# Performance work log

Hardware: AMD Instinct MI355X
Metric: run time of the kernel (lower is better)

The kernel has to match this reference:

```python
import jax, jax.numpy as jnp
import numpy as np

B, S, E, H = 2, 2048, 1024, 16
D = E // H  # head_dim = 64
FE = 4      # forward_expansion
EPS = 1e-5


def layernorm(x, g, b):
    mu = jnp.mean(x, axis=-1, keepdims=True)
    var = jnp.var(x, axis=-1, keepdims=True)
    return (x - mu) * jax.lax.rsqrt(var + EPS) * g + b


def setup_inputs() -> dict:
    key = jax.random.key(0)
    ks = jax.random.split(key, 16)
    s = lambda d: 1.0 / np.sqrt(d)
    return {
        "queries": jax.random.normal(ks[0], (B, S, E), jnp.float32),
        "keys": jax.random.normal(ks[1], (B, S, E), jnp.float32),
        "values": jax.random.normal(ks[2], (B, S, E), jnp.float32),
        "mask": jnp.ones((B, 1, S, S), jnp.int32),  # ignored (faithful to source bug)
        "Wq": jax.random.normal(ks[3], (D, D), jnp.float32) * s(D),
        "Wk": jax.random.normal(ks[4], (D, D), jnp.float32) * s(D),
        "Wv": jax.random.normal(ks[5], (D, D), jnp.float32) * s(D),
        "Wfc": jax.random.normal(ks[6], (E, E), jnp.float32) * s(E),
        "bfc": jnp.zeros((E,), jnp.float32),
        "W1": jax.random.normal(ks[7], (FE * E, E), jnp.float32) * s(E),
        "b1": jnp.zeros((FE * E,), jnp.float32),
        "W2": jax.random.normal(ks[8], (E, FE * E), jnp.float32) * s(FE * E),
        "b2": jnp.zeros((E,), jnp.float32),
        "ln1_g": jnp.ones((E,), jnp.float32),
        "ln1_b": jnp.zeros((E,), jnp.float32),
        "ln2_g": jnp.ones((E,), jnp.float32),
        "ln2_b": jnp.zeros((E,), jnp.float32),
    }


def reference(queries, keys, values, mask, Wq, Wk, Wv, Wfc, bfc, W1, b1, W2, b2,
              ln1_g, ln1_b, ln2_g, ln2_b):
    # --- MHA ---
    q = queries.reshape(B, S, H, D) @ Wq.T  # [B,S,H,D]
    k = keys.reshape(B, S, H, D) @ Wk.T
    v = values.reshape(B, S, H, D) @ Wv.T
    scores = jnp.einsum('bqhd,bkhd->bhqk', q, k)
    # source: softmax(scores / S**(-1/2)) == scores * sqrt(S)  (faithful quirk)
    # mask is ignored: source masked_fill is non-inplace and discarded
    attn = jax.nn.softmax(scores * jnp.sqrt(jnp.float32(S)), axis=-1)
    out = jnp.einsum('bhqk,bkhd->bqhd', attn, v).reshape(B, S, E)
    att = out @ Wfc.T + bfc
    # --- residual + LN + FFN + LN (dropout p=0 -> identity) ---
    h = layernorm(att + queries, ln1_g, ln1_b)
    x = jax.nn.relu(h @ W1.T + b1) @ W2.T + b2
    return layernorm(x + h, ln2_g, ln2_b)
```

## Files before the change

kernel.cpp:

```cpp
#include <hip/hip_runtime.h>
#include <hip/hip_bf16.h>
#include <math.h>

#define B_ 2
#define S_ 2048
#define E_ 1024
#define H_ 16
#define D_ 64
#define TOK (B_*S_)
#define SCALE 45.254833995939045f
#define SCALE2 (45.254833995939045f * 1.44269504088896340f)

typedef __bf16 bf16x8 __attribute__((ext_vector_type(8)));
typedef float floatx4 __attribute__((ext_vector_type(4)));
struct b4s { __hip_bfloat16 x, y, z, w; };

typedef const __attribute__((address_space(1))) char ga_char;
typedef __attribute__((address_space(3))) char ls_char;

__device__ __forceinline__ void gload_lds16(const void* g, ls_char* l) {
  __builtin_amdgcn_global_load_lds((ga_char*)g, l, 16, 0, 0);
}

#if __has_builtin(__builtin_amdgcn_exp2f)
#define EXP2(x) __builtin_amdgcn_exp2f(x)
#else
#define EXP2(x) exp2f(x)
#endif

#define SWZ(arr, half, row, qpos) \
  (*(bf16x8*)&arr[half][row][(((qpos) ^ ((row) & 3)) * 8)])

__device__ __forceinline__ int fsw(int r) {
  return ((r >> 3) & 1) | ((((r >> 4) ^ (r >> 2)) & 1) << 1);
}
#define SWZ2(arr, half, row, qpos) \
  (*(bf16x8*)&arr[half][row][(((qpos) ^ fsw(row)) * 8)])

__global__ __launch_bounds__(256) void cast_all(
    const float* __restrict__ Wfc, const float* __restrict__ W1,
    const float* __restrict__ W2, __hip_bfloat16* __restrict__ Wfcb,
    __hip_bfloat16* __restrict__ W1b, __hip_bfloat16* __restrict__ W2b,
    const float* __restrict__ Wq, const float* __restrict__ Wk,
    const float* __restrict__ Wv, __hip_bfloat16* __restrict__ Whl) {
  const int i = blockIdx.x * 256 + threadIdx.x;
  if (i < 2359296) {
    const float* src; __hip_bfloat16* dst; int j;
    if (i < 262144)       { src = Wfc; dst = Wfcb; j = i; }
    else if (i < 1310720) { src = W1;  dst = W1b;  j = i - 262144; }
    else                  { src = W2;  dst = W2b;  j = i - 1310720; }
    float4 v = ((const float4*)src)[j];
    b4s o;
    o.x = __float2bfloat16(v.x); o.y = __float2bfloat16(v.y);
    o.z = __float2bfloat16(v.z); o.w = __float2bfloat16(v.w);
    *(b4s*)(dst + (size_t)j * 4) = o;
  } else if (i < 2362368) {
    const int idx = i - 2359296;
    const int m = idx >> 10;
    const int off = (idx & 1023) * 4;
    const float* W = (m == 0) ? Wq : (m == 1) ? Wk : Wv;
    float4 v = *(const float4*)(W + off);
    b4s hi, lo;
    hi.x = __float2bfloat16(v.x); lo.x = __float2bfloat16(v.x - __bfloat162float(hi.x));
    hi.y = __float2bfloat16(v.y); lo.y = __float2bfloat16(v.y - __bfloat162float(hi.y));
    hi.z = __float2bfloat16(v.z); lo.z = __float2bfloat16(v.z - __bfloat162float(hi.z));
    hi.w = __float2bfloat16(v.w); lo.w = __float2bfloat16(v.w - __bfloat162float(hi.w));
    *(b4s*)(Whl + (size_t)m * 8192 + off) = hi;
    *(b4s*)(Whl + (size_t)m * 8192 + 4096 + off) = lo;
  }
}

__global__ __launch_bounds__(256) void qkv_fused(
    const float* __restrict__ xq, const float* __restrict__ xk,
    const float* __restrict__ xv, const __hip_bfloat16* __restrict__ Whl,
    __hip_bfloat16* __restrict__ qhi, __hip_bfloat16* __restrict__ qlo,
    __hip_bfloat16* __restrict__ khi, __hip_bfloat16* __restrict__ klo,
    __hip_bfloat16* __restrict__ vt) {
  __shared__ __bf16 Xh[2][64][32], Xl[2][64][32];
  __shared__ __bf16 Vt[64][72];
  const int t = threadIdx.x, lane = t & 63, w = t >> 6;
  const int quad = lane >> 4, low = lane & 15;
  const int bh = blockIdx.y;
  const int b = bh >> 4, h = bh & 15;
  const int s0 = blockIdx.x * 64;
  const int sr = t >> 2;
  const int sc = (t & 3) * 16;
  const int scc = sc >> 5;
  const int p0 = (sc & 31) >> 3;

  for (int m = 0; m < 3; m++) {
    const float* xin = (m == 0) ? xq : (m == 1) ? xk : xv;
    const __hip_bfloat16* Wh = Whl + (size_t)m * 8192;
    const float sc_m = (m == 0) ? SCALE2 : 1.0f;

    __syncthreads();
    {
      const float* src = xin + ((size_t)(b * S_ + s0 + sr)) * E_ + h * 64 + sc;
      float4 f0 = *(const float4*)(src);
      float4 f1 = *(const float4*)(src + 4);
      float4 f2 = *(const float4*)(src + 8);
      float4 f3 = *(const float4*)(src + 12);
      float fv[16] = {f0.x, f0.y, f0.z, f0.w, f1.x, f1.y, f1.z, f1.w,
                      f2.x, f2.y, f2.z, f2.w, f3.x, f3.y, f3.z, f3.w};
      bf16x8 hi0, hi1, lo0, lo1;
      #pragma unroll
      for (int j = 0; j < 8; j++) {
        hi0[j] = (__bf16)fv[j];
        lo0[j] = (__bf16)(fv[j] - (float)hi0[j]);
        hi1[j] = (__bf16)fv[8 + j];
        lo1[j] = (__bf16)(fv[8 + j] - (float)hi1[j]);
      }
      SWZ(Xh, scc, sr, p0) = hi0;
      SWZ(Xh, scc, sr, p0 + 1) = hi1;
      SWZ(Xl, scc, sr, p0) = lo0;
      SWZ(Xl, scc, sr, p0 + 1) = lo1;
    }
    __syncthreads();

    bf16x8 ah[2], al[2];
    #pragma unroll
    for (int c = 0; c < 2; c++) {
      ah[c] = SWZ(Xh, c, w * 16 + low, quad);
      al[c] = SWZ(Xl, c, w * 16 + low, quad);
    }

    floatx4 acc[4];
    #pragma unroll
    for (int nn = 0; nn < 4; nn++) {
      floatx4 a = {};
      #pragma unroll
      for (int c = 0; c < 2; c++) {
        const __hip_bfloat16* wp = Wh + (nn * 16 + low) * 64 + c * 32 + quad * 8;
        bf16x8 wh_ = *(const bf16x8*)wp;
        bf16x8 wl_ = *(const bf16x8*)(wp + 4096);
        a = __builtin_amdgcn_mfma_f32_16x16x32_bf16(ah[c], wh_, a, 0, 0, 0);
        a = __builtin_amdgcn_mfma_f32_16x16x32_bf16(al[c], wh_, a, 0, 0, 0);
        a = __builtin_amdgcn_mfma_f32_16x16x32_bf16(ah[c], wl_, a, 0, 0, 0);
      }
      acc[nn] = a;
    }

    if (m < 2) {
      __hip_bfloat16* dh = (m == 0) ? qhi : khi;
      __hip_bfloat16* dl = (m == 0) ? qlo : klo;
      #pragma unroll
      for (int nn = 0; nn < 4; nn++) {
        #pragma unroll
        for (int i = 0; i < 4; i++) {
          const int s = s0 + w * 16 + quad * 4 + i;
          const int d = nn * 16 + low;
          const size_t adr = ((size_t)bh * S_ + s) * 64 + d;
          const float f = acc[nn][i] * sc_m;
          const __hip_bfloat16 hb = __float2bfloat16(f);
          dh[adr] = hb;
          dl[adr] = __float2bfloat16(f - __bfloat162float(hb));
        }
      }
    } else {
      #pragma unroll
      for (int nn = 0; nn < 4; nn++)
        #pragma unroll
        for (int i = 0; i < 4; i++)
          Vt[nn * 16 + low][w * 16 + quad * 4 + i] = (__bf16)acc[nn][i];
      __syncthreads();
      const int dr = t >> 2;
      const int scl = (t & 3) * 16;
      __hip_bfloat16* dst = vt + ((size_t)bh * 64 + dr) * S_ + s0 + scl;
      bf16x8 o0 = *(const bf16x8*)&Vt[dr][scl];
      bf16x8 o1 = *(const bf16x8*)&Vt[dr][scl + 8];
      *(bf16x8*)dst = o0;
      *(bf16x8*)(dst + 8) = o1;
    }
  }
}

__global__ __launch_bounds__(512, 4) void attn_mfma(
    const __hip_bfloat16* __restrict__ Qhi, const __hip_bfloat16* __restrict__ Qlo,
    const __hip_bfloat16* __restrict__ Khi, const __hip_bfloat16* __restrict__ Klo,
    const __hip_bfloat16* __restrict__ Vtg, __hip_bfloat16* __restrict__ ctx) {
  __shared__ __bf16 Kh[2][2][64][32], Kl[2][2][64][32], Vs[2][2][64][32];
  const int t = threadIdx.x, lane = t & 63, w = t >> 6;
  const int quad = lane >> 4, low = lane & 15;
  const int bh = blockIdx.x;
  const int qw = blockIdx.y * 128 + w * 16;

  const int sh = w >> 2;
  const int r0 = (w & 3) * 16;
  const int srow = r0 + (lane >> 2);
  const int sq = (lane & 3) ^ fsw(srow);
  const __hip_bfloat16* gK = Khi + ((size_t)bh * S_ + srow) * 64 + sh * 32 + sq * 8;
  const __hip_bfloat16* gL = Klo + ((size_t)bh * S_ + srow) * 64 + sh * 32 + sq * 8;
  const __hip_bfloat16* gV = Vtg + ((size_t)bh * 64 + srow) * S_ + sh * 32 + sq * 8;

  bf16x8 qh[2], ql[2];
  {
    const size_t qbase = ((size_t)bh * S_ + qw + low) * 64 + quad * 8;
    qh[0] = *(const bf16x8*)(Qhi + qbase);
    qh[1] = *(const bf16x8*)(Qhi + qbase + 32);
    ql[0] = *(const bf16x8*)(Qlo + qbase);
    ql[1] = *(const bf16x8*)(Qlo + qbase + 32);
  }

  floatx4 oacc[4] = {};
  float mrow = -3e38f, lrow = 0.f;

  gload_lds16(gK, (ls_char*)&Kh[0][sh][r0][0]);
  gload_lds16(gL, (ls_char*)&Kl[0][sh][r0][0]);
  gload_lds16(gV, (ls_char*)&Vs[0][sh][r0][0]);

  for (int kt = 0; kt < S_ / 64; kt++) {
    const int cur = kt & 1;
    __syncthreads();
    if (kt + 1 < S_ / 64) {
      gload_lds16(gK + (size_t)(kt + 1) * 4096, (ls_char*)&Kh[cur ^ 1][sh][r0][0]);
      gload_lds16(gL + (size_t)(kt + 1) * 4096, (ls_char*)&Kl[cur ^ 1][sh][r0][0]);
      gload_lds16(gV + (size_t)(kt + 1) * 64,   (ls_char*)&Vs[cur ^ 1][sh][r0][0]);
    }

    floatx4 sa[4];
    #pragma unroll
    for (int nn = 0; nn < 4; nn++) {
      const int prow = (nn & 1) * 32 + (nn >> 1) * 4 + (low >> 2) * 8 + (low & 3);
      bf16x8 kh0 = SWZ2(Kh[cur], 0, prow, quad);
      bf16x8 kh1 = SWZ2(Kh[cur], 1, prow, quad);
      bf16x8 kl0 = SWZ2(Kl[cur], 0, prow, quad);
      bf16x8 kl1 = SWZ2(Kl[cur], 1, prow, quad);
      floatx4 s = {};
      s = __builtin_amdgcn_mfma_f32_16x16x32_bf16(kh0, qh[0], s, 0, 0, 0);
      s = __builtin_amdgcn_mfma_f32_16x16x32_bf16(kh1, qh[1], s, 0, 0, 0);
      s = __builtin_amdgcn_mfma_f32_16x16x32_bf16(kl0, qh[0], s, 0, 0, 0);
      s = __builtin_amdgcn_mfma_f32_16x16x32_bf16(kl1, qh[1], s, 0, 0, 0);
      s = __builtin_amdgcn_mfma_f32_16x16x32_bf16(kh0, ql[0], s, 0, 0, 0);
      s = __builtin_amdgcn_mfma_f32_16x16x32_bf16(kh1, ql[1], s, 0, 0, 0);
      sa[nn] = s;
    }

    float rmax;
    {
      float m0 = fmaxf(fmaxf(sa[0][0], sa[0][1]), fmaxf(sa[0][2], sa[0][3]));
      float m1 = fmaxf(fmaxf(sa[1][0], sa[1][1]), fmaxf(sa[1][2], sa[1][3]));
      float m2 = fmaxf(fmaxf(sa[2][0], sa[2][1]), fmaxf(sa[2][2], sa[2][3]));
      float m3 = fmaxf(fmaxf(sa[3][0], sa[3][1]), fmaxf(sa[3][2], sa[3][3]));
      rmax = fmaxf(fmaxf(m0, m1), fmaxf(m2, m3));
      rmax = fmaxf(rmax, __shfl_xor(rmax, 16, 64));
      rmax = fmaxf(rmax, __shfl_xor(rmax, 32, 64));
    }
    if (__any(rmax > mrow)) {
      const float nm = fmaxf(mrow, rmax);
      const float al = EXP2(mrow - nm);
      mrow = nm;
      lrow *= al;
      #pragma unroll
      for (int dt = 0; dt < 4; dt++) {
        oacc[dt][0] *= al; oacc[dt][1] *= al;
        oacc[dt][2] *= al; oacc[dt][3] *= al;
      }
    }
    float p[4][4];
    float rs;
    {
      float r0_ = 0.f, r1_ = 0.f, r2_ = 0.f, r3_ = 0.f;
      #pragma unroll
      for (int i = 0; i < 4; i++) {
        p[0][i] = EXP2(sa[0][i] - mrow); r0_ += p[0][i];
        p[1][i] = EXP2(sa[1][i] - mrow); r1_ += p[1][i];
        p[2][i] = EXP2(sa[2][i] - mrow); r2_ += p[2][i];
        p[3][i] = EXP2(sa[3][i] - mrow); r3_ += p[3][i];
      }
      rs = (r0_ + r1_) + (r2_ + r3_);
      rs += __shfl_xor(rs, 16, 64);
      rs += __shfl_xor(rs, 32, 64);
    }
    lrow += rs;

    bf16x8 pb[2];
    #pragma unroll
    for (int kh2 = 0; kh2 < 2; kh2++) {
      bf16x8 v;
      v[0] = (__bf16)p[kh2][0]; v[1] = (__bf16)p[kh2][1];
      v[2] = (__bf16)p[kh2][2]; v[3] = (__bf16)p[kh2][3];
      v[4] = (__bf16)p[kh2 + 2][0]; v[5] = (__bf16)p[kh2 + 2][1];
      v[6] = (__bf16)p[kh2 + 2][2]; v[7] = (__bf16)p[kh2 + 2][3];
      pb[kh2] = v;
    }

    #pragma unroll
    for (int dt = 0; dt < 4; dt++) {
      bf16x8 vb0 = SWZ2(Vs[cur], 0, dt * 16 + low, quad);
      bf16x8 vb1 = SWZ2(Vs[cur], 1, dt * 16 + low, quad);
      oacc[dt] = __builtin_amdgcn_mfma_f32_16x16x32_bf16(vb0, pb[0], oacc[dt], 0, 0, 0);
      oacc[dt] = __builtin_amdgcn_mfma_f32_16x16x32_bf16(vb1, pb[1], oacc[dt], 0, 0, 0);
    }
  }

  const float inv = 1.0f / lrow;
  const int b = bh >> 4, h = bh & 15;
  const size_t base = ((size_t)(b * S_ + qw + low)) * E_ + h * 64 + quad * 4;
  #pragma unroll
  for (int dt = 0; dt < 4; dt++) {
    b4s o;
    o.x = __float2bfloat16(oacc[dt][0] * inv);
    o.y = __float2bfloat16(oacc[dt][1] * inv);
    o.z = __float2bfloat16(oacc[dt][2] * inv);
    o.w = __float2bfloat16(oacc[dt][3] * inv);
    *(b4s*)(ctx + base + dt * 16) = o;
  }
}

template <int RELU, int OUT_BF16, int PARTIAL>
__global__ __launch_bounds__(256) void gemm_mfma(
    const __hip_bfloat16* __restrict__ A, const __hip_bfloat16* __restrict__ Wt,
    const float* __restrict__ bias, void* __restrict__ C0, void* __restrict__ C1,
    int M, int N, int Kblk, int lda) {
  __shared__ __bf16 As[128][64];
  __shared__ __bf16 Bs[128][64];
  const int t = threadIdx.x;
  const int lane = t & 63;
  const int w = t >> 6;
  const int wr = w >> 1, wc = w & 1;
  const int m0 = blockIdx.y * 128, n0 = blockIdx.x * 128;
  void* Cout = (blockIdx.z == 0) ? C0 : C1;

  A += (size_t)blockIdx.z * Kblk;
  Wt += (size_t)blockIdx.z * Kblk;

  floatx4 acc[4][4] = {};
  const int srow = t >> 3;
  const int ssc = ((t & 7) ^ (srow & 7)) * 8;

  const __hip_bfloat16* gA = A + (size_t)(m0 + srow) * lda + ssc;
  const __hip_bfloat16* gB = Wt + (size_t)(n0 + srow) * lda + ssc;
  ls_char* lA = (ls_char*)&As[0][0] + w * 1024;
  ls_char* lB = (ls_char*)&Bs[0][0] + w * 1024;
  const size_t rstep = (size_t)32 * lda;

  for (int k0 = 0; k0 < Kblk; k0 += 64) {
    __syncthreads();
    gload_lds16(gA + k0,             lA);
    gload_lds16(gA + k0 + rstep,     lA + 4096);
    gload_lds16(gA + k0 + 2 * rstep, lA + 8192);
    gload_lds16(gA + k0 + 3 * rstep, lA + 12288);
    gload_lds16(gB + k0,             lB);
    gload_lds16(gB + k0 + rstep,     lB + 4096);
    gload_lds16(gB + k0 + 2 * rstep, lB + 8192);
    gload_lds16(gB + k0 + 3 * rstep, lB + 12288);
    __syncthreads();

    #pragma unroll
    for (int ks = 0; ks < 2; ks++) {
      bf16x8 af[4], bfr[4];
      #pragma unroll
      for (int i = 0; i < 4; i++) {
        const int ra = wr * 64 + i * 16 + (lane & 15);
        const int ca = (((lane >> 4) + ks * 4) ^ (ra & 7)) * 8;
        af[i] = *(const bf16x8*)&As[ra][ca];
        const int rb = wc * 64 + i * 16 + (lane & 15);
        const int cb = (((lane >> 4) + ks * 4) ^ (rb & 7)) * 8;
        bfr[i] = *(const bf16x8*)&Bs[rb][cb];
      }
      #pragma unroll
      for (int mi = 0; mi < 4; mi++)
        #pragma unroll
        for (int ni = 0; ni < 4; ni++)
          acc[mi][ni] = __builtin_amdgcn_mfma_f32_16x16x32_bf16(
              af[mi], bfr[ni], acc[mi][ni], 0, 0, 0);
    }
  }

  const int cil = lane & 15;
  const int quad = lane >> 4;
  #pragma unroll
  for (int ni = 0; ni < 4; ni++) {
    const int col = n0 + wc * 64 + ni * 16 + cil;
    const float bb = PARTIAL ? 0.f : bias[col];
    #pragma unroll
    for (int mi = 0; mi < 4; mi++) {
      const int row = m0 + wr * 64 + mi * 16 + quad * 4;
      #pragma unroll
      for (int i = 0; i < 4; i++) {
        if (PARTIAL) {
          ((float*)Cout)[(size_t)(row + i) * N + col] = acc[mi][ni][i];
        } else {
          float vv = acc[mi][ni][i] + bb;
          if (RELU) vv = fmaxf(vv, 0.f);
          if (OUT_BF16)
            ((__hip_bfloat16*)Cout)[(size_t)(row + i) * N + col] = __float2bfloat16(vv);
          else
            ((float*)Cout)[(size_t)(row + i) * N + col] = vv;
        }
      }
    }
  }
}

template <int EMIT_BF16>
__global__ __launch_bounds__(256) void add_ln(
    const float* __restrict__ a0, const float* __restrict__ a1,
    const float* __restrict__ r, const float* __restrict__ bias,
    const float* __restrict__ g, const float* __restrict__ bt,
    float* __restrict__ out, __hip_bfloat16* __restrict__ outb) {
  __shared__ float red[16];
  const int tok = blockIdx.x, t = threadIdx.x;
  float4 av = ((const float4*)(a0 + (size_t)tok * E_))[t];
  float4 a2 = ((const float4*)(a1 + (size_t)tok * E_))[t];
  float4 rv = ((const float4*)(r + (size_t)tok * E_))[t];
  float4 cv = ((const float4*)bias)[t];
  float4 x;
  x.x = av.x + a2.x + rv.x + cv.x; x.y = av.y + a2.y + rv.y + cv.y;
  x.z = av.z + a2.z + rv.z + cv.z; x.w = av.w + a2.w + rv.w + cv.w;
  float sum = x.x + x.y + x.z + x.w;
  float ssq = x.x * x.x + x.y * x.y + x.z * x.z + x.w * x.w;
  #pragma unroll
  for (int off = 32; off >= 1; off >>= 1) {
    sum += __shfl_down(sum, off, 64);
    ssq += __shfl_down(ssq, off, 64);
  }
  const int wave = t >> 6;
  if ((t & 63) == 0) { red[wave] = sum; red[4 + wave] = ssq; }
  __syncthreads();
  if (t == 0) {
    float s = red[0] + red[1] + red[2] + red[3];
    float qq = red[4] + red[5] + red[6] + red[7];
    float mu = s * (1.0f / E_);
    red[8] = mu;
    red[9] = qq * (1.0f / E_) - mu * mu;
  }
  __syncthreads();
  const float mu = red[8];
  const float inv = rsqrtf(red[9] + 1e-5f);
  float4 gv = ((const float4*)g)[t];
  float4 bv = ((const float4*)bt)[t];
  float4 o;
  o.x = (x.x - mu) * inv * gv.x + bv.x;
  o.y = (x.y - mu) * inv * gv.y + bv.y;
  o.z = (x.z - mu) * inv * gv.z + bv.z;
  o.w = (x.w - mu) * inv * gv.w + bv.w;
  ((float4*)(out + (size_t)tok * E_))[t] = o;
  if (EMIT_BF16) {
    b4s ob;
    ob.x = __float2bfloat16(o.x); ob.y = __float2bfloat16(o.y);
    ob.z = __float2bfloat16(o.z); ob.w = __float2bfloat16(o.w);
    *(b4s*)(outb + (size_t)tok * E_ + t * 4) = ob;
  }
}

extern "C" void kernel_launch(void* const* d_in, const int* in_sizes, int n_in,
                              void* d_out, int out_size, void* d_ws, size_t ws_size,
                              hipStream_t stream) {
  const float* queries = (const float*)d_in[0];
  const float* keys    = (const float*)d_in[1];
  const float* values  = (const float*)d_in[2];
  const float* Wq  = (const float*)d_in[4];
  const float* Wk  = (const float*)d_in[5];
  const float* Wv  = (const float*)d_in[6];
  const float* Wfc = (const float*)d_in[7];
  const float* bfc = (const float*)d_in[8];
  const float* W1  = (const float*)d_in[9];
  const float* b1  = (const float*)d_in[10];
  const float* W2  = (const float*)d_in[11];
  const float* b2  = (const float*)d_in[12];
  const float* ln1_g = (const float*)d_in[13];
  const float* ln1_b = (const float*)d_in[14];
  const float* ln2_g = (const float*)d_in[15];
  const float* ln2_b = (const float*)d_in[16];

  const size_t M1 = 1048576;
  float* ws = (float*)d_ws;
  float* P0  = ws;
  float* P1  = ws + 4 * M1;
  float* Hf  = ws + 8 * M1;
  __hip_bfloat16* bb = (__hip_bfloat16*)(ws + 12 * M1);
  __hip_bfloat16* CTXb = bb;
  __hip_bfloat16* Hb   = bb + 4 * M1;
  __hip_bfloat16* Wfcb = bb + 8 * M1;
  __hip_bfloat16* W1b  = bb + 9 * M1;
  __hip_bfloat16* W2b  = bb + 13 * M1;
  __hip_bfloat16* Qhi  = bb + 17 * M1;
  __hip_bfloat16* Qlo  = bb + 21 * M1;
  __hip_bfloat16* Khi  = bb + 25 * M1;
  __hip_bfloat16* Klo  = bb + 29 * M1;
  __hip_bfloat16* Vtb  = bb + 33 * M1;
  __hip_bfloat16* FF1b = bb + 17 * M1;
  __hip_bfloat16* Whlb = bb + 37 * M1;
  float* out = (float*)d_out;

  cast_all<<<9228, 256, 0, stream>>>(Wfc, W1, W2, Wfcb, W1b, W2b,
                                     Wq, Wk, Wv, Whlb);

  qkv_fused<<<dim3(S_ / 64, B_ * H_), 256, 0, stream>>>(
      queries, keys, values, Whlb, Qhi, Qlo, Khi, Klo, Vtb);
  attn_mfma<<<dim3(B_ * H_, S_ / 128), 512, 0, stream>>>(
      Qhi, Qlo, Khi, Klo, Vtb, CTXb);
  gemm_mfma<0, 0, 1><<<dim3(E_ / 128, TOK / 128, 2), 256, 0, stream>>>(
      CTXb, Wfcb, nullptr, P0, P1, TOK, E_, 512, E_);
  add_ln<1><<<TOK, 256, 0, stream>>>(P0, P1, queries, bfc, ln1_g, ln1_b, Hf, Hb);
  gemm_mfma<1, 1, 0><<<dim3(4 * E_ / 128, TOK / 128, 1), 256, 0, stream>>>(
      Hb, W1b, b1, FF1b, FF1b, TOK, 4 * E_, E_, E_);
  gemm_mfma<0, 0, 1><<<dim3(E_ / 128, TOK / 128, 2), 256, 0, stream>>>(
      FF1b, W2b, nullptr, P0, P1, TOK, E_, 2048, 4 * E_);
  add_ln<0><<<TOK, 256, 0, stream>>>(P0, P1, Hf, b2, ln2_g, ln2_b, out, nullptr);
}
```

Baseline: 397.2 us.

## Add MFMA priority hints, simplify LDS swizzle, drop split-K for Wfc GEMM

The attention kernel raises wave priority around its MFMA blocks with s_setprio and moves the softmax into a helper. It also replaces the custom fsw LDS swizzle with the simpler row&3 XOR swizzle, which may bring back bank conflicts. The output-projection GEMM no longer uses split-K: it runs as one pass with bias fused in, so the first add_ln reads one partial instead of two plus bias. add_ln is templated to skip loads it does not need.

```diff
diff --git a/kernel.cpp b/kernel.cpp
--- a/kernel.cpp
+++ b/kernel.cpp
@@ -8,7 +8,6 @@
 #define H_ 16
 #define D_ 64
 #define TOK (B_*S_)
-#define SCALE 45.254833995939045f
 #define SCALE2 (45.254833995939045f * 1.44269504088896340f)
 
 typedef __bf16 bf16x8 __attribute__((ext_vector_type(8)));
@@ -30,12 +29,6 @@
 
 #define SWZ(arr, half, row, qpos) \
   (*(bf16x8*)&arr[half][row][(((qpos) ^ ((row) & 3)) * 8)])
-
-__device__ __forceinline__ int fsw(int r) {
-  return ((r >> 3) & 1) | ((((r >> 4) ^ (r >> 2)) & 1) << 1);
-}
-#define SWZ2(arr, half, row, qpos) \
-  (*(bf16x8*)&arr[half][row][(((qpos) ^ fsw(row)) * 8)])
 
 __global__ __launch_bounds__(256) void cast_all(
     const float* __restrict__ Wfc, const float* __restrict__ W1,
@@ -174,6 +167,56 @@
   }
 }
 
+__device__ __forceinline__ void softmax_update(
+    const floatx4* sa, floatx4* oacc, float& mrow, float& lrow, bf16x8* pb) {
+  float rmax;
+  {
+    float m0 = fmaxf(fmaxf(sa[0][0], sa[0][1]), fmaxf(sa[0][2], sa[0][3]));
+    float m1 = fmaxf(fmaxf(sa[1][0], sa[1][1]), fmaxf(sa[1][2], sa[1][3]));
+    float m2 = fmaxf(fmaxf(sa[2][0], sa[2][1]), fmaxf(sa[2][2], sa[2][3]));
+    float m3 = fmaxf(fmaxf(sa[3][0], sa[3][1]), fmaxf(sa[3][2], sa[3][3]));
+    rmax = fmaxf(fmaxf(m0, m1), fmaxf(m2, m3));
+    rmax = fmaxf(rmax, __shfl_xor(rmax, 16, 64));
+    rmax = fmaxf(rmax, __shfl_xor(rmax, 32, 64));
+  }
+  if (__any(rmax > mrow)) {
+    const float nm = fmaxf(mrow, rmax);
+    const float al = EXP2(mrow - nm);
+    mrow = nm;
+    lrow *= al;
+    #pragma unroll
+    for (int dt = 0; dt < 4; dt++) {
+      oacc[dt][0] *= al; oacc[dt][1] *= al;
+      oacc[dt][2] *= al; oacc[dt][3] *= al;
+    }
+  }
+  float p[4][4];
+  float rs;
+  {
+    float r0_ = 0.f, r1_ = 0.f, r2_ = 0.f, r3_ = 0.f;
+    #pragma unroll
+    for (int i = 0; i < 4; i++) {
+      p[0][i] = EXP2(sa[0][i] - mrow); r0_ += p[0][i];
+      p[1][i] = EXP2(sa[1][i] - mrow); r1_ += p[1][i];
+      p[2][i] = EXP2(sa[2][i] - mrow); r2_ += p[2][i];
+      p[3][i] = EXP2(sa[3][i] - mrow); r3_ += p[3][i];
+    }
+    rs = (r0_ + r1_) + (r2_ + r3_);
+    rs += __shfl_xor(rs, 16, 64);
+    rs += __shfl_xor(rs, 32, 64);
+  }
+  lrow += rs;
+  #pragma unroll
+  for (int kh2 = 0; kh2 < 2; kh2++) {
+    bf16x8 v;
+    v[0] = (__bf16)p[kh2][0]; v[1] = (__bf16)p[kh2][1];
+    v[2] = (__bf16)p[kh2][2]; v[3] = (__bf16)p[kh2][3];
+    v[4] = (__bf16)p[kh2 + 2][0]; v[5] = (__bf16)p[kh2 + 2][1];
+    v[6] = (__bf16)p[kh2 + 2][2]; v[7] = (__bf16)p[kh2 + 2][3];
+    pb[kh2] = v;
+  }
+}
+
 __global__ __launch_bounds__(512, 4) void attn_mfma(
     const __hip_bfloat16* __restrict__ Qhi, const __hip_bfloat16* __restrict__ Qlo,
     const __hip_bfloat16* __restrict__ Khi, const __hip_bfloat16* __restrict__ Klo,
@@ -187,7 +230,7 @@
   const int sh = w >> 2;
   const int r0 = (w & 3) * 16;
   const int srow = r0 + (lane >> 2);
-  const int sq = (lane & 3) ^ fsw(srow);
+  const int sq = (lane & 3) ^ (srow & 3);
   const __hip_bfloat16* gK = Khi + ((size_t)bh * S_ + srow) * 64 + sh * 32 + sq * 8;
   const __hip_bfloat16* gL = Klo + ((size_t)bh * S_ + srow) * 64 + sh * 32 + sq * 8;
   const __hip_bfloat16* gV = Vtg + ((size_t)bh * 64 + srow) * S_ + sh * 32 + sq * 8;
@@ -218,13 +261,14 @@
     }
 
     floatx4 sa[4];
+    __builtin_amdgcn_s_setprio(1);
     #pragma unroll
     for (int nn = 0; nn < 4; nn++) {
       const int prow = (nn & 1) * 32 + (nn >> 1) * 4 + (low >> 2) * 8 + (low & 3);
-      bf16x8 kh0 = SWZ2(Kh[cur], 0, prow, quad);
-      bf16x8 kh1 = SWZ2(Kh[cur], 1, prow, quad);
-      bf16x8 kl0 = SWZ2(Kl[cur], 0, prow, quad);
-      bf16x8 kl1 = SWZ2(Kl[cur], 1, prow, quad);
+      bf16x8 kh0 = SWZ(Kh[cur], 0, prow, quad);
+      bf16x8 kh1 = SWZ(Kh[cur], 1, prow, quad);
+      bf16x8 kl0 = SWZ(Kl[cur], 0, prow, quad);
+      bf16x8 kl1 = SWZ(Kl[cur], 1, prow, quad);
       floatx4 s = {};
       s = __builtin_amdgcn_mfma_f32_16x16x32_bf16(kh0, qh[0], s, 0, 0, 0);
       s = __builtin_amdgcn_mfma_f32_16x16x32_bf16(kh1, qh[1], s, 0, 0, 0);
@@ -234,63 +278,20 @@
       s = __builtin_amdgcn_mfma_f32_16x16x32_bf16(kh1, ql[1], s, 0, 0, 0);
       sa[nn] = s;
     }
-
-    float rmax;
-    {
-      float m0 = fmaxf(fmaxf(sa[0][0], sa[0][1]), fmaxf(sa[0][2], sa[0][3]));
-      float m1 = fmaxf(fmaxf(sa[1][0], sa[1][1]), fmaxf(sa[1][2], sa[1][3]));
-      float m2 = fmaxf(fmaxf(sa[2][0], sa[2][1]), fmaxf(sa[2][2], sa[2][3]));
-      float m3 = fmaxf(fmaxf(sa[3][0], sa[3][1]), fmaxf(sa[3][2], sa[3][3]));
-      rmax = fmaxf(fmaxf(m0, m1), fmaxf(m2, m3));
-      rmax = fmaxf(rmax, __shfl_xor(rmax, 16, 64));
-      rmax = fmaxf(rmax, __shfl_xor(rmax, 32, 64));
-    }
-    if (__any(rmax > mrow)) {
-      const float nm = fmaxf(mrow, rmax);
-      const float al = EXP2(mrow - nm);
-      mrow = nm;
-      lrow *= al;
-      #pragma unroll
-      for (int dt = 0; dt < 4; dt++) {
-        oacc[dt][0] *= al; oacc[dt][1] *= al;
-        oacc[dt][2] *= al; oacc[dt][3] *= al;
-      }
-    }
-    float p[4][4];
-    float rs;
-    {
-      float r0_ = 0.f, r1_ = 0.f, r2_ = 0.f, r3_ = 0.f;
-      #pragma unroll
-      for (int i = 0; i < 4; i++) {
-        p[0][i] = EXP2(sa[0][i] - mrow); r0_ += p[0][i];
-        p[1][i] = EXP2(sa[1][i] - mrow); r1_ += p[1][i];
-        p[2][i] = EXP2(sa[2][i] - mrow); r2_ += p[2][i];
-        p[3][i] = EXP2(sa[3][i] - mrow); r3_ += p[3][i];
-      }
-      rs = (r0_ + r1_) + (r2_ + r3_);
-      rs += __shfl_xor(rs, 16, 64);
-      rs += __shfl_xor(rs, 32, 64);
-    }
-    lrow += rs;
+    __builtin_amdgcn_s_setprio(0);
 
     bf16x8 pb[2];
-    #pragma unroll
-    for (int kh2 = 0; kh2 < 2; kh2++) {
-      bf16x8 v;
-      v[0] = (__bf16)p[kh2][0]; v[1] = (__bf16)p[kh2][1];
-      v[2] = (__bf16)p[kh2][2]; v[3] = (__bf16)p[kh2][3];
-      v[4] = (__bf16)p[kh2 + 2][0]; v[5] = (__bf16)p[kh2 + 2][1];
-      v[6] = (__bf16)p[kh2 + 2][2]; v[7] = (__bf16)p[kh2 + 2][3];
-      pb[kh2] = v;
-    }
-
+    softmax_update(sa, oacc, mrow, lrow, pb);
+
+    __builtin_amdgcn_s_setprio(1);
     #pragma unroll
     for (int dt = 0; dt < 4; dt++) {
-      bf16x8 vb0 = SWZ2(Vs[cur], 0, dt * 16 + low, quad);
-      bf16x8 vb1 = SWZ2(Vs[cur], 1, dt * 16 + low, quad);
+      bf16x8 vb0 = SWZ(Vs[cur], 0, dt * 16 + low, quad);
+      bf16x8 vb1 = SWZ(Vs[cur], 1, dt * 16 + low, quad);
       oacc[dt] = __builtin_amdgcn_mfma_f32_16x16x32_bf16(vb0, pb[0], oacc[dt], 0, 0, 0);
       oacc[dt] = __builtin_amdgcn_mfma_f32_16x16x32_bf16(vb1, pb[1], oacc[dt], 0, 0, 0);
     }
+    __builtin_amdgcn_s_setprio(0);
   }
 
   const float inv = 1.0f / lrow;
@@ -393,7 +394,7 @@
   }
 }
 
-template <int EMIT_BF16>
+template <int EMIT_BF16, int HAS_A1, int HAS_BIAS>
 __global__ __launch_bounds__(256) void add_ln(
     const float* __restrict__ a0, const float* __restrict__ a1,
     const float* __restrict__ r, const float* __restrict__ bias,
@@ -402,12 +403,17 @@
   __shared__ float red[16];
   const int tok = blockIdx.x, t = threadIdx.x;
   float4 av = ((const float4*)(a0 + (size_t)tok * E_))[t];
-  float4 a2 = ((const float4*)(a1 + (size_t)tok * E_))[t];
   float4 rv = ((const float4*)(r + (size_t)tok * E_))[t];
-  float4 cv = ((const float4*)bias)[t];
   float4 x;
-  x.x = av.x + a2.x + rv.x + cv.x; x.y = av.y + a2.y + rv.y + cv.y;
-  x.z = av.z + a2.z + rv.z + cv.z; x.w = av.w + a2.w + rv.w + cv.w;
+  x.x = av.x + rv.x; x.y = av.y + rv.y; x.z = av.z + rv.z; x.w = av.w + rv.w;
+  if (HAS_A1) {
+    float4 a2 = ((const float4*)(a1 + (size_t)tok * E_))[t];
+    x.x += a2.x; x.y += a2.y; x.z += a2.z; x.w += a2.w;
+  }
+  if (HAS_BIAS) {
+    float4 cv = ((const float4*)bias)[t];
+    x.x += cv.x; x.y += cv.y; x.z += cv.z; x.w += cv.w;
+  }
   float sum = x.x + x.y + x.z + x.w;
   float ssq = x.x * x.x + x.y * x.y + x.z * x.z + x.w * x.w;
   #pragma unroll
@@ -491,12 +497,14 @@
       queries, keys, values, Whlb, Qhi, Qlo, Khi, Klo, Vtb);
   attn_mfma<<<dim3(B_ * H_, S_ / 128), 512, 0, stream>>>(
       Qhi, Qlo, Khi, Klo, Vtb, CTXb);
-  gemm_mfma<0, 0, 1><<<dim3(E_ / 128, TOK / 128, 2), 256, 0, stream>>>(
-      CTXb, Wfcb, nullptr, P0, P1, TOK, E_, 512, E_);
-  add_ln<1><<<TOK, 256, 0, stream>>>(P0, P1, queries, bfc, ln1_g, ln1_b, Hf, Hb);
+  gemm_mfma<0, 0, 0><<<dim3(E_ / 128, TOK / 128, 1), 256, 0, stream>>>(
+      CTXb, Wfcb, bfc, P0, nullptr, TOK, E_, E_, E_);
+  add_ln<1, 0, 0><<<TOK, 256, 0, stream>>>(
+      P0, nullptr, queries, nullptr, ln1_g, ln1_b, Hf, Hb);
   gemm_mfma<1, 1, 0><<<dim3(4 * E_ / 128, TOK / 128, 1), 256, 0, stream>>>(
-      Hb, W1b, b1, FF1b, FF1b, TOK, 4 * E_, E_, E_);
+      Hb, W1b, b1, FF1b, nullptr, TOK, 4 * E_, E_, E_);
   gemm_mfma<0, 0, 1><<<dim3(E_ / 128, TOK / 128, 2), 256, 0, stream>>>(
       FF1b, W2b, nullptr, P0, P1, TOK, E_, 2048, 4 * E_);
-  add_ln<0><<<TOK, 256, 0, stream>>>(P0, P1, Hf, b2, ln2_g, ln2_b, out, nullptr);
-}
+  add_ln<0, 1, 1><<<TOK, 256, 0, stream>>>(
+      P0, P1, Hf, b2, ln2_g, ln2_b, out, nullptr);
+}
```

Result: no change. 399.7 us (+0.6%).
